# Kernel tuning notes

Measured on AMD Instinct MI355X. Metric: run time of the kernel, lower is better.

## Reference

```python
import jax, jax.numpy as jnp
import numpy as np

N = 50000      # nodes
E = 800000     # edges (avg degree 16)
D = 128        # in_dim = hidden_dim
C = 40         # num_classes
BN_EPS = 1e-5


def setup_inputs() -> dict:
    key = jax.random.key(0)
    ks = jax.random.split(key, 24)
    h = jax.random.normal(ks[0], (N, D), dtype=jnp.float32)
    edge_src = jax.random.randint(ks[1], (E,), 0, N)
    edge_dst = jax.random.randint(ks[2], (E,), 0, N)
    mask = jnp.ones((E, 1), dtype=jnp.float32)  # adj_mask2_fixed (frozen)

    def lin_w(k, fi, fo):
        return jax.random.normal(k, (fi, fo), dtype=jnp.float32) / np.sqrt(fi).astype(np.float32)

    def lin_b(k, fo):
        return jax.random.normal(k, (fo,), dtype=jnp.float32) * 0.01

    dims = [(D, D), (D, D), (D, C)]  # last GIN layer -> num_classes
    out = {"h": h, "edge_src": edge_src, "edge_dst": edge_dst, "mask": mask}
    for i, (fi, fo) in enumerate(dims):
        out[f"w{i}"] = lin_w(ks[3 + 4 * i], fi, fo)
        out[f"b{i}"] = lin_b(ks[4 + 4 * i], fo)
        out[f"g{i}"] = jnp.ones((fo,), jnp.float32) + 0.05 * jax.random.normal(ks[5 + 4 * i], (fo,), jnp.float32)
        out[f"beta{i}"] = 0.05 * jax.random.normal(ks[6 + 4 * i], (fo,), jnp.float32)
        out[f"rm{i}"] = 0.1 * jax.random.normal(jax.random.fold_in(key, 100 + i), (fo,), jnp.float32)
        out[f"rv{i}"] = jax.random.uniform(jax.random.fold_in(key, 200 + i), (fo,), jnp.float32, 0.5, 1.5)
    out["wp"] = lin_w(ks[20], D, C)
    out["bp"] = lin_b(ks[21], C)
    return out


def reference(h, edge_src, edge_dst, mask,
              w0, b0, g0, beta0, rm0, rv0,
              w1, b1, g1, beta1, rm1, rv1,
              w2, b2, g2, beta2, rm2, rv2,
              wp, bp):
    # in-degree for mean aggregation (DGL mean reducer: divide by in-degree,
    # zero for isolated nodes)
    ones_e = jnp.ones(edge_dst.shape, dtype=h.dtype)
    deg = jax.ops.segment_sum(ones_e, edge_dst, num_segments=N)
    deg_inv = jnp.where(deg > 0, 1.0 / jnp.maximum(deg, 1.0), 0.0)[:, None]

    def gin_layer(x, w, b, g, beta, rm, rv):
        msg = x[edge_src] * mask                                   # [E, d]
        agg = jax.ops.segment_sum(msg, edge_dst, num_segments=N) * deg_inv
        z = (x + agg) @ w + b                                      # (1+eps)=1, eps=0
        z = (z - rm) * jax.lax.rsqrt(rv + BN_EPS) * g + beta       # BN (eval, running stats)
        return jax.nn.relu(z)                                      # dropout: eval -> identity

    h1 = gin_layer(h, w0, b0, g0, beta0, rm0, rv0)    # [N, D]
    h2 = gin_layer(h1, w1, b1, g1, beta1, rm1, rv1)   # [N, D]  hidden_rep[-2]
    h3 = gin_layer(h2, w2, b2, g2, beta2, rm2, rv2)   # [N, C]  hidden_rep[-1]
    return ((h2 @ wp + bp) + h3) * 0.5
```

## Files before the change

### kernel.cpp

```cpp
#include <hip/hip_runtime.h>

#define N_NODES 50000
#define N_EDGES 800000
#define DIM 128
#define NCLS 40
#define N_PAD 50432
#define NPB 197

typedef __bf16 bf16x8_t __attribute__((ext_vector_type(8)));
typedef unsigned short us8_t __attribute__((ext_vector_type(8)));
typedef float f32x4_t __attribute__((ext_vector_type(4)));

static __device__ __forceinline__ float b2f(unsigned short h) {
    unsigned u = ((unsigned)h) << 16;
    return __builtin_bit_cast(float, u);
}
static __device__ __forceinline__ unsigned short f2b(float f) {
    unsigned u = __builtin_bit_cast(unsigned, f);
    u += 0x7FFFu + ((u >> 16) & 1u);
    return (unsigned short)(u >> 16);
}

#define PREP_B 3125
#define REPACK_B 176
#define DEG_B 200
__global__ __launch_bounds__(256) void prep(const float* __restrict__ hsrc,
                                            unsigned short* __restrict__ hout,
                                            const float* __restrict__ w0,
                                            const float* __restrict__ w1,
                                            const float* __restrict__ w2,
                                            const float* __restrict__ wp,
                                            unsigned short* __restrict__ f0h,
                                            unsigned short* __restrict__ f0l,
                                            unsigned short* __restrict__ f1h,
                                            unsigned short* __restrict__ f1l,
                                            unsigned short* __restrict__ f2h,
                                            unsigned short* __restrict__ f2l,
                                            unsigned short* __restrict__ fph,
                                            unsigned short* __restrict__ fpl,
                                            const int* __restrict__ edst,
                                            int* __restrict__ deg) {
    if (blockIdx.x < PREP_B) {
        size_t e0 = ((size_t)blockIdx.x * 256 + threadIdx.x) * 8;
        f32x4_t v0 = *(const f32x4_t*)(hsrc + e0);
        f32x4_t v1 = *(const f32x4_t*)(hsrc + e0 + 4);
        us8_t o;
        #pragma unroll
        for (int j = 0; j < 4; ++j) { o[j] = f2b(v0[j]); o[4 + j] = f2b(v1[j]); }
        *(us8_t*)(hout + e0) = o;
        return;
    }
    if (blockIdx.x >= PREP_B + REPACK_B) {
        int t0 = (blockIdx.x - PREP_B - REPACK_B) * 256 + threadIdx.x;
        for (int e = t0; e < N_EDGES; e += DEG_B * 256)
            atomicAdd(&deg[edst[e]], 1);
        return;
    }
    int t = (blockIdx.x - PREP_B) * 256 + threadIdx.x;
    const float* src;
    unsigned short *dh, *dl;
    int idx, ncols;
    if (t < 16384)      { src = w0; dh = f0h; dl = f0l; idx = t;         ncols = 128; }
    else if (t < 32768) { src = w1; dh = f1h; dl = f1l; idx = t - 16384; ncols = 128; }
    else if (t < 38912) { src = w2; dh = f2h; dl = f2l; idx = t - 32768; ncols = 48; }
    else if (t < 45056) { src = wp; dh = fph; dl = fpl; idx = t - 38912; ncols = 48; }
    else return;
    int k = idx / ncols, n = idx - k * ncols;
    float v;
    if (ncols == 128) v = src[k * 128 + n];
    else              v = (n < NCLS) ? src[k * NCLS + n] : 0.f;
    int nt = n >> 4, m = n & 15, kt = k >> 5, quad = (k >> 3) & 3, j = k & 7;
    int off = ((nt * 4 + kt) * 64 + quad * 16 + m) * 8 + j;
    unsigned short hi = f2b(v);
    dh[off] = hi;
    dl[off] = f2b(v - b2f(hi));
}

__global__ __launch_bounds__(256) void deg_partial(const int* __restrict__ deg,
                                                   int* __restrict__ partial) {
    __shared__ int lds[256];
    int n = blockIdx.x * 256 + threadIdx.x;
    lds[threadIdx.x] = (n < N_NODES) ? deg[n] : 0;
    __syncthreads();
    #pragma unroll
    for (int off = 128; off > 0; off >>= 1) {
        if (threadIdx.x < off) lds[threadIdx.x] += lds[threadIdx.x + off];
        __syncthreads();
    }
    if (threadIdx.x == 0) partial[blockIdx.x] = lds[0];
}

__global__ __launch_bounds__(256) void deg_scan(const int* __restrict__ deg,
                                                const int* __restrict__ partial,
                                                int* __restrict__ rs,
                                                int* __restrict__ cur,
                                                float* __restrict__ dinv) {
    __shared__ int lds[256];
    int b = blockIdx.x, tid = threadIdx.x;
    lds[tid] = (tid < b) ? partial[tid] : 0;
    __syncthreads();
    #pragma unroll
    for (int off = 128; off > 0; off >>= 1) {
        if (tid < off) lds[tid] += lds[tid + off];
        __syncthreads();
    }
    int boff = lds[0];
    __syncthreads();
    int n = b * 256 + tid;
    int d = (n < N_NODES) ? deg[n] : 0;
    lds[tid] = d;
    __syncthreads();
    #pragma unroll
    for (int off = 1; off < 256; off <<= 1) {
        int v = lds[tid];
        int add = (tid >= off) ? lds[tid - off] : 0;
        __syncthreads();
        lds[tid] = v + add;
        __syncthreads();
    }
    if (n < N_NODES) {
        int excl = boff + lds[tid] - d;
        rs[n] = excl;
        cur[n] = excl;
        dinv[n] = (d > 0) ? (1.0f / (float)d) : 0.0f;
    }
}

__global__ __launch_bounds__(256) void fill_atomic(const int* __restrict__ esrc,
                                                   const int* __restrict__ edst,
                                                   const float* __restrict__ mask,
                                                   int* __restrict__ cur,
                                                   unsigned* __restrict__ csr) {
    int e = blockIdx.x * 256 + threadIdx.x;
    if (e >= N_EDGES) return;
    int d = edst[e];
    int s = esrc[e];
    float mk = mask[e];
    int slot = atomicAdd(&cur[d], 1);
    csr[slot] = (unsigned)s | ((unsigned)f2b(mk) << 16);
}

static __device__ __forceinline__ void issue16(const unsigned short* __restrict__ xb,
                                               unsigned pk, int lane, unsigned* vv) {
    #pragma unroll
    for (int j = 0; j < 16; ++j) {
        unsigned p = (unsigned)__builtin_amdgcn_readlane((int)pk, j);
        vv[j] = *(const unsigned*)(xb + (size_t)(p & 0xFFFFu) * DIM + lane * 2);
    }
}
static __device__ __forceinline__ void accum16(unsigned pk, const unsigned* vv,
                                               float& acc0, float& acc1) {
    #pragma unroll
    for (int j = 0; j < 16; ++j) {
        unsigned p = (unsigned)__builtin_amdgcn_readlane((int)pk, j);
        float mm = b2f((unsigned short)(p >> 16));
        acc0 += mm * b2f((unsigned short)(vv[j] & 0xFFFFu));
        acc1 += mm * b2f((unsigned short)(vv[j] >> 16));
    }
}

static __device__ __forceinline__ void gather4(const unsigned short* __restrict__ xb,
                                               const float* __restrict__ xres,
                                               const int* __restrict__ rs,
                                               const int* __restrict__ deg,
                                               const float* __restrict__ dinv,
                                               const unsigned* __restrict__ csr,
                                               int nb0, int lane,
                                               float (*ldsrow)[132], int row0) {
    int rs4[4], dg4[4];
    float di4[4];
    #pragma unroll
    for (int i = 0; i < 4; ++i) {
        int n = nb0 + i;
        rs4[i] = rs[n];
        dg4[i] = deg[n];
        di4[i] = dinv[n];
    }
    unsigned pk0, pk1, pk2, pk3;
    pk0 = (lane < (dg4[0] < 16 ? dg4[0] : 16)) ? csr[rs4[0] + lane] : 0u;
    pk1 = (lane < (dg4[1] < 16 ? dg4[1] : 16)) ? csr[rs4[1] + lane] : 0u;

    unsigned vvA[16], vvB[16];
    issue16(xb, pk0, lane, vvA);

    unsigned pkq[4] = {pk0, pk1, 0u, 0u};
    #pragma unroll
    for (int i = 0; i < 4; ++i) {
        if (i == 0) pk2 = (lane < (dg4[2] < 16 ? dg4[2] : 16)) ? csr[rs4[2] + lane] : 0u;
        if (i == 1) pk3 = (lane < (dg4[3] < 16 ? dg4[3] : 16)) ? csr[rs4[3] + lane] : 0u;
        if (i == 0) pkq[2] = pk2;
        if (i == 1) pkq[3] = pk3;
        if (i < 3) issue16(xb, pkq[i + 1], lane, (i & 1) ? vvA : vvB);
        float acc0 = 0.f, acc1 = 0.f;
        accum16(pkq[i], (i & 1) ? vvB : vvA, acc0, acc1);
        for (int base = 16; base < dg4[i]; base += 16) {
            int nb = dg4[i] - base;
            if (nb > 16) nb = 16;
            unsigned pke = (lane < nb) ? csr[rs4[i] + base + lane] : 0u;
            unsigned vvE[16];
            issue16(xb, pke, lane, vvE);
            accum16(pke, vvE, acc0, acc1);
        }
        float di = di4[i];
        float2 xp = *(const float2*)(xres + (size_t)(nb0 + i) * DIM + lane * 2);
        ldsrow[row0 + i][lane * 2]     = xp.x + acc0 * di;
        ldsrow[row0 + i][lane * 2 + 1] = xp.y + acc1 * di;
    }
}

__global__ __launch_bounds__(256) void fused_layer(const unsigned short* __restrict__ xb,
                                                   const float* __restrict__ x,
                                                   const int* __restrict__ rs,
                                                   const int* __restrict__ deg,
                                                   const float* __restrict__ dinv,
                                                   const unsigned* __restrict__ csr,
                                                   const unsigned short* __restrict__ wfh,
                                                   const unsigned short* __restrict__ wfl,
                                                   const float* __restrict__ bias,
                                                   const float* __restrict__ gam,
                                                   const float* __restrict__ bet,
                                                   const float* __restrict__ rm,
                                                   const float* __restrict__ rv,
                                                   float* __restrict__ out,
                                                   unsigned short* __restrict__ outb) {
    __shared__ float lds[16][132];
    int tid = threadIdx.x;
    int wave = tid >> 6, lane = tid & 63;
    int rbase = blockIdx.x * 16;

    gather4(xb, x, rs, deg, dinv, csr, rbase + wave * 4, lane, lds, wave * 4);
    __syncthreads();

    int m = lane & 15, quad = lane >> 4;
    const float* ap = &lds[m][0];

    us8_t ah[4], al[4];
    #pragma unroll
    for (int kt = 0; kt < 4; ++kt) {
        f32x4_t p0 = *(const f32x4_t*)(ap + kt * 32 + quad * 8);
        f32x4_t p1 = *(const f32x4_t*)(ap + kt * 32 + quad * 8 + 4);
        #pragma unroll
        for (int j = 0; j < 4; ++j) {
            unsigned short h0 = f2b(p0[j]);
            unsigned short h1 = f2b(p1[j]);
            ah[kt][j] = h0;
            ah[kt][4 + j] = h1;
            al[kt][j] = f2b(p0[j] - b2f(h0));
            al[kt][4 + j] = f2b(p1[j] - b2f(h1));
        }
    }

    f32x4_t acc[2] = {};
    #pragma unroll
    for (int kt = 0; kt < 4; ++kt) {
        #pragma unroll
        for (int t = 0; t < 2; ++t) {
            int nt = wave * 2 + t;
            int boff = ((nt * 4 + kt) * 64 + lane) * 8;
            us8_t bh = *(const us8_t*)(wfh + boff);
            us8_t bl = *(const us8_t*)(wfl + boff);
            acc[t] = __builtin_amdgcn_mfma_f32_16x16x32_bf16(
                __builtin_bit_cast(bf16x8_t, ah[kt]),
                __builtin_bit_cast(bf16x8_t, bh), acc[t], 0, 0, 0);
            acc[t] = __builtin_amdgcn_mfma_f32_16x16x32_bf16(
                __builtin_bit_cast(bf16x8_t, ah[kt]),
                __builtin_bit_cast(bf16x8_t, bl), acc[t], 0, 0, 0);
            acc[t] = __builtin_amdgcn_mfma_f32_16x16x32_bf16(
                __builtin_bit_cast(bf16x8_t, al[kt]),
                __builtin_bit_cast(bf16x8_t, bh), acc[t], 0, 0, 0);
        }
    }

    #pragma unroll
    for (int t = 0; t < 2; ++t) {
        int nt = wave * 2 + t;
        int j = nt * 16 + m;
        float bj = bias[j];
        float sc = gam[j] * rsqrtf(rv[j] + 1e-5f);
        float sh = bet[j] - rm[j] * sc;
        #pragma unroll
        for (int i = 0; i < 4; ++i) {
            int r = rbase + quad * 4 + i;
            float z = fmaxf((acc[t][i] + bj) * sc + sh, 0.f);
            out[(size_t)r * DIM + j] = z;
            outb[(size_t)r * DIM + j] = f2b(z);
        }
    }
}

__global__ __launch_bounds__(256) void fused_final2(const unsigned short* __restrict__ xb,
                                                    const float* __restrict__ h2,
                                                    const int* __restrict__ rs,
                                                    const int* __restrict__ deg,
                                                    const float* __restrict__ dinv,
                                                    const unsigned* __restrict__ csr,
                                                    const unsigned short* __restrict__ f2h,
                                                    const unsigned short* __restrict__ f2l,
                                                    const unsigned short* __restrict__ fph,
                                                    const unsigned short* __restrict__ fpl,
                                                    const float* __restrict__ b2,
                                                    const float* __restrict__ g2,
                                                    const float* __restrict__ be2,
                                                    const float* __restrict__ rm2,
                                                    const float* __restrict__ rv2,
                                                    const float* __restrict__ bp,
                                                    float* __restrict__ out) {
    __shared__ float lds[16][132];
    int tid = threadIdx.x;
    int wave = tid >> 6, lane = tid & 63;
    int rbase = blockIdx.x * 16;

    gather4(xb, h2, rs, deg, dinv, csr, rbase + wave * 4, lane, lds, wave * 4);
    __syncthreads();

    if (wave == 3) return;

    int m = lane & 15, quad = lane >> 4;
    int arow = rbase + m;
    const float* ap2 = &lds[m][0];
    const float* aph = h2 + (size_t)arow * DIM;

    us8_t a2h[4], a2l[4], ahh[4], ahl[4];
    #pragma unroll
    for (int kt = 0; kt < 4; ++kt) {
        f32x4_t p0 = *(const f32x4_t*)(ap2 + kt * 32 + quad * 8);
        f32x4_t p1 = *(const f32x4_t*)(ap2 + kt * 32 + quad * 8 + 4);
        f32x4_t q0 = *(const f32x4_t*)(aph + kt * 32 + quad * 8);
        f32x4_t q1 = *(const f32x4_t*)(aph + kt * 32 + quad * 8 + 4);
        #pragma unroll
        for (int j = 0; j < 4; ++j) {
            unsigned short h0 = f2b(p0[j]), h1 = f2b(p1[j]);
            a2h[kt][j] = h0; a2h[kt][4 + j] = h1;
            a2l[kt][j] = f2b(p0[j] - b2f(h0));
            a2l[kt][4 + j] = f2b(p1[j] - b2f(h1));
            unsigned short g0 = f2b(q0[j]), g1 = f2b(q1[j]);
            ahh[kt][j] = g0; ahh[kt][4 + j] = g1;
            ahl[kt][j] = f2b(q0[j] - b2f(g0));
            ahl[kt][4 + j] = f2b(q1[j] - b2f(g1));
        }
    }

    int nt = wave;
    f32x4_t acc2 = {};
    f32x4_t accp = {};
    #pragma unroll
    for (int kt = 0; kt < 4; ++kt) {
        int boff = ((nt * 4 + kt) * 64 + lane) * 8;
        us8_t b2hv = *(const us8_t*)(f2h + boff);
        us8_t b2lv = *(const us8_t*)(f2l + boff);
        us8_t bphv = *(const us8_t*)(fph + boff);
        us8_t bplv = *(const us8_t*)(fpl + boff);
        acc2 = __builtin_amdgcn_mfma_f32_16x16x32_bf16(
            __builtin_bit_cast(bf16x8_t, a2h[kt]),
            __builtin_bit_cast(bf16x8_t, b2hv), acc2, 0, 0, 0);
        acc2 = __builtin_amdgcn_mfma_f32_16x16x32_bf16(
            __builtin_bit_cast(bf16x8_t, a2h[kt]),
            __builtin_bit_cast(bf16x8_t, b2lv), acc2, 0, 0, 0);
        acc2 = __builtin_amdgcn_mfma_f32_16x16x32_bf16(
            __builtin_bit_cast(bf16x8_t, a2l[kt]),
            __builtin_bit_cast(bf16x8_t, b2hv), acc2, 0, 0, 0);
        accp = __builtin_amdgcn_mfma_f32_16x16x32_bf16(
            __builtin_bit_cast(bf16x8_t, ahh[kt]),
            __builtin_bit_cast(bf16x8_t, bphv), accp, 0, 0, 0);
        accp = __builtin_amdgcn_mfma_f32_16x16x32_bf16(
            __builtin_bit_cast(bf16x8_t, ahh[kt]),
            __builtin_bit_cast(bf16x8_t, bplv), accp, 0, 0, 0);
        accp = __builtin_amdgcn_mfma_f32_16x16x32_bf16(
            __builtin_bit_cast(bf16x8_t, ahl[kt]),
            __builtin_bit_cast(bf16x8_t, bphv), accp, 0, 0, 0);
    }

    int j = nt * 16 + m;
    if (j < NCLS) {
        float b2j = b2[j];
        float sc = g2[j] * rsqrtf(rv2[j] + 1e-5f);
        float sh = be2[j] - rm2[j] * sc;
        float bpj = bp[j];
        #pragma unroll
        for (int i = 0; i < 4; ++i) {
            int r = rbase + quad * 4 + i;
            float z = fmaxf((acc2[i] + b2j) * sc + sh, 0.f);
            float p = accp[i] + bpj;
            out[(size_t)r * NCLS + j] = (p + z) * 0.5f;
        }
    }
}

extern "C" void kernel_launch(void* const* d_in, const int* in_sizes, int n_in,
                              void* d_out, int out_size, void* d_ws, size_t ws_size,
                              hipStream_t stream) {
    const float* h    = (const float*)d_in[0];
    const int* esrc   = (const int*)d_in[1];
    const int* edst   = (const int*)d_in[2];
    const float* mask = (const float*)d_in[3];
    const float* w0   = (const float*)d_in[4];
    const float* b0   = (const float*)d_in[5];
    const float* g0   = (const float*)d_in[6];
    const float* be0  = (const float*)d_in[7];
    const float* rm0  = (const float*)d_in[8];
    const float* rv0  = (const float*)d_in[9];
    const float* w1   = (const float*)d_in[10];
    const float* b1   = (const float*)d_in[11];
    const float* g1   = (const float*)d_in[12];
    const float* be1  = (const float*)d_in[13];
    const float* rm1  = (const float*)d_in[14];
    const float* rv1  = (const float*)d_in[15];
    const float* w2   = (const float*)d_in[16];
    const float* b2   = (const float*)d_in[17];
    const float* g2   = (const float*)d_in[18];
    const float* be2  = (const float*)d_in[19];
    const float* rm2  = (const float*)d_in[20];
    const float* rv2  = (const float*)d_in[21];
    const float* wp   = (const float*)d_in[22];
    const float* bp   = (const float*)d_in[23];

    char* ws = (char*)d_ws;
    size_t off = 0;
    auto alloc = [&](size_t bytes) {
        char* p = ws + off;
        off = (off + bytes + 255) & ~(size_t)255;
        return p;
    };
    int* rs       = (int*)alloc(N_PAD * 4);
    int* deg      = (int*)alloc(N_PAD * 4);
    int* cur      = (int*)alloc(N_PAD * 4);
    float* dinv   = (float*)alloc(N_PAD * 4);
    int* partial  = (int*)alloc(256 * 4);
    unsigned* csr = (unsigned*)alloc((size_t)N_EDGES * 4);
    float* hbA    = (float*)alloc((size_t)N_NODES * DIM * 4);
    float* hbB    = (float*)alloc((size_t)N_NODES * DIM * 4);
    unsigned short* xb16  = (unsigned short*)alloc((size_t)N_NODES * DIM * 2);
    unsigned short* hbA16 = (unsigned short*)alloc((size_t)N_NODES * DIM * 2);
    unsigned short* hbB16 = (unsigned short*)alloc((size_t)N_NODES * DIM * 2);
    unsigned short* f0h = (unsigned short*)alloc(16384 * 2);
    unsigned short* f0l = (unsigned short*)alloc(16384 * 2);
    unsigned short* f1h = (unsigned short*)alloc(16384 * 2);
    unsigned short* f1l = (unsigned short*)alloc(16384 * 2);
    unsigned short* f2h = (unsigned short*)alloc(6144 * 2);
    unsigned short* f2l = (unsigned short*)alloc(6144 * 2);
    unsigned short* fph = (unsigned short*)alloc(6144 * 2);
    unsigned short* fpl = (unsigned short*)alloc(6144 * 2);

    const int GB16 = N_NODES / 16;

    hipMemsetAsync(deg, 0, N_NODES * 4, stream);
    prep<<<PREP_B + REPACK_B + DEG_B, 256, 0, stream>>>(
        h, xb16, w0, w1, w2, wp,
        f0h, f0l, f1h, f1l, f2h, f2l, fph, fpl, edst, deg);
    deg_partial<<<NPB, 256, 0, stream>>>(deg, partial);
    deg_scan<<<NPB, 256, 0, stream>>>(deg, partial, rs, cur, dinv);
    fill_atomic<<<(N_EDGES + 255) / 256, 256, 0, stream>>>(esrc, edst, mask, cur, csr);

    fused_layer<<<GB16, 256, 0, stream>>>(xb16, h, rs, deg, dinv, csr,
                                          f0h, f0l, b0, g0, be0, rm0, rv0, hbA, hbA16);
    fused_layer<<<GB16, 256, 0, stream>>>(hbA16, hbA, rs, deg, dinv, csr,
                                          f1h, f1l, b1, g1, be1, rm1, rv1, hbB, hbB16);
    fused_final2<<<GB16, 256, 0, stream>>>(hbB16, hbB, rs, deg, dinv, csr,
                                           f2h, f2l, fph, fpl,
                                           b2, g2, be2, rm2, rv2, bp, (float*)d_out);
}
```

Before: 345.4 us.

## Store hidden activations as bf16 hi/lo pairs instead of fp32 plus bf16

Intermediate layer outputs are now written as a bf16 high part and a bf16 residual low part, replacing the previous fp32 copy plus bf16 copy. The residual term and the final layer's A-operand are rebuilt from the hi/lo pair, which cuts bytes written and read per layer and removes the fp32-to-bf16 split in the final kernel. Separately, the degree count switches from a grid-stride loop to one edge per thread with more blocks. Reconstruction from hi+lo is slightly less exact than fp32.

```diff
diff --git a/kernel.cpp b/kernel.cpp
--- a/kernel.cpp
+++ b/kernel.cpp
@@ -23,7 +23,7 @@
 
 #define PREP_B 3125
 #define REPACK_B 176
-#define DEG_B 200
+#define DEGC_B 3125
 __global__ __launch_bounds__(256) void prep(const float* __restrict__ hsrc,
                                             unsigned short* __restrict__ hout,
                                             const float* __restrict__ w0,
@@ -51,9 +51,8 @@
         return;
     }
     if (blockIdx.x >= PREP_B + REPACK_B) {
-        int t0 = (blockIdx.x - PREP_B - REPACK_B) * 256 + threadIdx.x;
-        for (int e = t0; e < N_EDGES; e += DEG_B * 256)
-            atomicAdd(&deg[edst[e]], 1);
+        int e = (blockIdx.x - PREP_B - REPACK_B) * 256 + threadIdx.x;
+        atomicAdd(&deg[edst[e]], 1);
         return;
     }
     int t = (blockIdx.x - PREP_B) * 256 + threadIdx.x;
@@ -159,8 +158,10 @@
     }
 }
 
+template<bool RES32>
 static __device__ __forceinline__ void gather4(const unsigned short* __restrict__ xb,
                                                const float* __restrict__ xres,
+                                               const unsigned short* __restrict__ xlo,
                                                const int* __restrict__ rs,
                                                const int* __restrict__ deg,
                                                const float* __restrict__ dinv,
@@ -202,14 +203,25 @@
             accum16(pke, vvE, acc0, acc1);
         }
         float di = di4[i];
-        float2 xp = *(const float2*)(xres + (size_t)(nb0 + i) * DIM + lane * 2);
-        ldsrow[row0 + i][lane * 2]     = xp.x + acc0 * di;
-        ldsrow[row0 + i][lane * 2 + 1] = xp.y + acc1 * di;
-    }
-}
-
+        float x0, x1;
+        if constexpr (RES32) {
+            float2 xp = *(const float2*)(xres + (size_t)(nb0 + i) * DIM + lane * 2);
+            x0 = xp.x; x1 = xp.y;
+        } else {
+            unsigned hv = *(const unsigned*)(xb  + (size_t)(nb0 + i) * DIM + lane * 2);
+            unsigned lv = *(const unsigned*)(xlo + (size_t)(nb0 + i) * DIM + lane * 2);
+            x0 = b2f((unsigned short)(hv & 0xFFFFu)) + b2f((unsigned short)(lv & 0xFFFFu));
+            x1 = b2f((unsigned short)(hv >> 16))     + b2f((unsigned short)(lv >> 16));
+        }
+        ldsrow[row0 + i][lane * 2]     = x0 + acc0 * di;
+        ldsrow[row0 + i][lane * 2 + 1] = x1 + acc1 * di;
+    }
+}
+
+template<bool RES32>
 __global__ __launch_bounds__(256) void fused_layer(const unsigned short* __restrict__ xb,
-                                                   const float* __restrict__ x,
+                                                   const float* __restrict__ xres,
+                                                   const unsigned short* __restrict__ xlo,
                                                    const int* __restrict__ rs,
                                                    const int* __restrict__ deg,
                                                    const float* __restrict__ dinv,
@@ -221,14 +233,14 @@
                                                    const float* __restrict__ bet,
                                                    const float* __restrict__ rm,
                                                    const float* __restrict__ rv,
-                                                   float* __restrict__ out,
-                                                   unsigned short* __restrict__ outb) {
+                                                   unsigned short* __restrict__ outhi,
+                                                   unsigned short* __restrict__ outlo) {
     __shared__ float lds[16][132];
     int tid = threadIdx.x;
     int wave = tid >> 6, lane = tid & 63;
     int rbase = blockIdx.x * 16;
 
-    gather4(xb, x, rs, deg, dinv, csr, rbase + wave * 4, lane, lds, wave * 4);
+    gather4<RES32>(xb, xres, xlo, rs, deg, dinv, csr, rbase + wave * 4, lane, lds, wave * 4);
     __syncthreads();
 
     int m = lane & 15, quad = lane >> 4;
@@ -282,14 +294,15 @@
         for (int i = 0; i < 4; ++i) {
             int r = rbase + quad * 4 + i;
             float z = fmaxf((acc[t][i] + bj) * sc + sh, 0.f);
-            out[(size_t)r * DIM + j] = z;
-            outb[(size_t)r * DIM + j] = f2b(z);
+            unsigned short zh = f2b(z);
+            outhi[(size_t)r * DIM + j] = zh;
+            outlo[(size_t)r * DIM + j] = f2b(z - b2f(zh));
         }
     }
 }
 
 __global__ __launch_bounds__(256) void fused_final2(const unsigned short* __restrict__ xb,
-                                                    const float* __restrict__ h2,
+                                                    const unsigned short* __restrict__ xlo,
                                                     const int* __restrict__ rs,
                                                     const int* __restrict__ deg,
                                                     const float* __restrict__ dinv,
@@ -310,7 +323,7 @@
     int wave = tid >> 6, lane = tid & 63;
     int rbase = blockIdx.x * 16;
 
-    gather4(xb, h2, rs, deg, dinv, csr, rbase + wave * 4, lane, lds, wave * 4);
+    gather4<false>(xb, nullptr, xlo, rs, deg, dinv, csr, rbase + wave * 4, lane, lds, wave * 4);
     __syncthreads();
 
     if (wave == 3) return;
@@ -318,25 +331,22 @@
     int m = lane & 15, quad = lane >> 4;
     int arow = rbase + m;
     const float* ap2 = &lds[m][0];
-    const float* aph = h2 + (size_t)arow * DIM;
+    const unsigned short* aphh = xb  + (size_t)arow * DIM;
+    const unsigned short* aphl = xlo + (size_t)arow * DIM;
 
     us8_t a2h[4], a2l[4], ahh[4], ahl[4];
     #pragma unroll
     for (int kt = 0; kt < 4; ++kt) {
         f32x4_t p0 = *(const f32x4_t*)(ap2 + kt * 32 + quad * 8);
         f32x4_t p1 = *(const f32x4_t*)(ap2 + kt * 32 + quad * 8 + 4);
-        f32x4_t q0 = *(const f32x4_t*)(aph + kt * 32 + quad * 8);
-        f32x4_t q1 = *(const f32x4_t*)(aph + kt * 32 + quad * 8 + 4);
+        ahh[kt] = *(const us8_t*)(aphh + kt * 32 + quad * 8);
+        ahl[kt] = *(const us8_t*)(aphl + kt * 32 + quad * 8);
         #pragma unroll
         for (int j = 0; j < 4; ++j) {
             unsigned short h0 = f2b(p0[j]), h1 = f2b(p1[j]);
             a2h[kt][j] = h0; a2h[kt][4 + j] = h1;
             a2l[kt][j] = f2b(p0[j] - b2f(h0));
             a2l[kt][4 + j] = f2b(p1[j] - b2f(h1));
-            unsigned short g0 = f2b(q0[j]), g1 = f2b(q1[j]);
-            ahh[kt][j] = g0; ahh[kt][4 + j] = g1;
-            ahl[kt][j] = f2b(q0[j] - b2f(g0));
-            ahl[kt][4 + j] = f2b(q1[j] - b2f(g1));
         }
     }
 
@@ -427,11 +437,11 @@
     float* dinv   = (float*)alloc(N_PAD * 4);
     int* partial  = (int*)alloc(256 * 4);
     unsigned* csr = (unsigned*)alloc((size_t)N_EDGES * 4);
-    float* hbA    = (float*)alloc((size_t)N_NODES * DIM * 4);
-    float* hbB    = (float*)alloc((size_t)N_NODES * DIM * 4);
-    unsigned short* xb16  = (unsigned short*)alloc((size_t)N_NODES * DIM * 2);
-    unsigned short* hbA16 = (unsigned short*)alloc((size_t)N_NODES * DIM * 2);
-    unsigned short* hbB16 = (unsigned short*)alloc((size_t)N_NODES * DIM * 2);
+    unsigned short* xb16   = (unsigned short*)alloc((size_t)N_NODES * DIM * 2);
+    unsigned short* hbA_hi = (unsigned short*)alloc((size_t)N_NODES * DIM * 2);
+    unsigned short* hbA_lo = (unsigned short*)alloc((size_t)N_NODES * DIM * 2);
+    unsigned short* hbB_hi = (unsigned short*)alloc((size_t)N_NODES * DIM * 2);
+    unsigned short* hbB_lo = (unsigned short*)alloc((size_t)N_NODES * DIM * 2);
     unsigned short* f0h = (unsigned short*)alloc(16384 * 2);
     unsigned short* f0l = (unsigned short*)alloc(16384 * 2);
     unsigned short* f1h = (unsigned short*)alloc(16384 * 2);
@@ -444,18 +454,20 @@
     const int GB16 = N_NODES / 16;
 
     hipMemsetAsync(deg, 0, N_NODES * 4, stream);
-    prep<<<PREP_B + REPACK_B + DEG_B, 256, 0, stream>>>(
+    prep<<<PREP_B + REPACK_B + DEGC_B, 256, 0, stream>>>(
         h, xb16, w0, w1, w2, wp,
         f0h, f0l, f1h, f1l, f2h, f2l, fph, fpl, edst, deg);
     deg_partial<<<NPB, 256, 0, stream>>>(deg, partial);
     deg_scan<<<NPB, 256, 0, stream>>>(deg, partial, rs, cur, dinv);
     fill_atomic<<<(N_EDGES + 255) / 256, 256, 0, stream>>>(esrc, edst, mask, cur, csr);
 
-    fused_layer<<<GB16, 256, 0, stream>>>(xb16, h, rs, deg, dinv, csr,
-                                          f0h, f0l, b0, g0, be0, rm0, rv0, hbA, hbA16);
-    fused_layer<<<GB16, 256, 0, stream>>>(hbA16, hbA, rs, deg, dinv, csr,
-                                          f1h, f1l, b1, g1, be1, rm1, rv1, hbB, hbB16);
-    fused_final2<<<GB16, 256, 0, stream>>>(hbB16, hbB, rs, deg, dinv, csr,
+    fused_layer<true><<<GB16, 256, 0, stream>>>(xb16, h, xb16, rs, deg, dinv, csr,
+                                                f0h, f0l, b0, g0, be0, rm0, rv0,
+                                                hbA_hi, hbA_lo);
+    fused_layer<false><<<GB16, 256, 0, stream>>>(hbA_hi, h, hbA_lo, rs, deg, dinv, csr,
+                                                 f1h, f1l, b1, g1, be1, rm1, rv1,
+                                                 hbB_hi, hbB_lo);
+    fused_final2<<<GB16, 256, 0, stream>>>(hbB_hi, hbB_lo, rs, deg, dinv, csr,
                                            f2h, f2l, fph, fpl,
                                            b2, g2, be2, rm2, rv2, bp, (float*)d_out);
 }
```

New measurement: 331.2 us. 1.04x faster.
